# Performance work log

Measured on AMD Instinct MI355X. Metric: run time of the kernel, lower is better.

Reference implementation:

```python
import jax, jax.numpy as jnp
import numpy as np

N = 40000      # num nodes
E = 640000     # num edges (avg degree 16)
R = 4          # num relations
F = 128        # num_node_features
EMB = 128      # embedding_size
HID = 256      # hidden_size
V = 16         # direction_vocab_size
B = 4096       # number of (nest, food) queries


def setup_inputs() -> dict:
    key = jax.random.key(0)
    ks = jax.random.split(key, 17)
    s = 0.05
    return {
        "x": jax.random.normal(ks[0], (N, F), jnp.float32),
        "edge_index": jax.random.randint(ks[1], (2, E), 0, N, dtype=jnp.int32),
        "edge_type": jax.random.randint(ks[2], (E,), 0, R, dtype=jnp.int32),
        "nest_tensor": jax.random.randint(ks[3], (B,), 0, N, dtype=jnp.int32),
        "food_tensor": jax.random.randint(ks[4], (B,), 0, N, dtype=jnp.int32),
        # RGCN layer 1 (F -> EMB)
        "Wrel1": jax.random.normal(ks[5], (R, F, EMB), jnp.float32) * s,
        "Wroot1": jax.random.normal(ks[6], (F, EMB), jnp.float32) * s,
        "b1": jnp.zeros((EMB,), jnp.float32),
        # RGCN layer 2 (EMB -> EMB)
        "Wrel2": jax.random.normal(ks[7], (R, EMB, EMB), jnp.float32) * s,
        "Wroot2": jax.random.normal(ks[8], (EMB, EMB), jnp.float32) * s,
        "b2": jnp.zeros((EMB,), jnp.float32),
        # MLP heads
        "fc_W": jax.random.normal(ks[9], (2 * EMB, HID), jnp.float32) * s,
        "fc_b": jnp.zeros((HID,), jnp.float32),
        "dir_W": jax.random.normal(ks[10], (HID, V), jnp.float32) * s,
        "dir_b": jnp.zeros((V,), jnp.float32),
        "dist_W": jax.random.normal(ks[11], (HID, 1), jnp.float32) * s,
        "dist_b": jnp.zeros((1,), jnp.float32),
    }


def rgcn_conv(x, edge_index, edge_type, Wrel, Wroot, b, num_nodes):
    """PyG-style RGCNConv: root transform + per-relation mean-aggregated messages."""
    src, dst = edge_index[0], edge_index[1]
    out = x @ Wroot + b                                   # [N, H]
    num_rel = Wrel.shape[0]
    for r in range(num_rel):                              # small fixed loop over relations
        mask = (edge_type == r)
        xr = x @ Wrel[r]                                  # [N, H] transform-then-gather
        msg = jnp.where(mask[:, None], xr[src], 0.0)      # [E, H]
        agg = jax.ops.segment_sum(msg, dst, num_segments=num_nodes)
        cnt = jax.ops.segment_sum(mask.astype(x.dtype), dst, num_segments=num_nodes)
        out = out + agg / jnp.maximum(cnt, 1.0)[:, None]  # mean per relation per node
    return out


def reference(x, edge_index, edge_type, nest_tensor, food_tensor,
              Wrel1, Wroot1, b1, Wrel2, Wroot2, b2,
              fc_W, fc_b, dir_W, dir_b, dist_W, dist_b):
    num_nodes = x.shape[0]
    h = jax.nn.relu(rgcn_conv(x, edge_index, edge_type, Wrel1, Wroot1, b1, num_nodes))
    h = rgcn_conv(h, edge_index, edge_type, Wrel2, Wroot2, b2, num_nodes)
    combined = jnp.concatenate([h[nest_tensor], h[food_tensor]], axis=-1)  # [B, 2*EMB]
    hidden = jax.nn.relu(combined @ fc_W + fc_b)                           # [B, HID]
    token_a = jax.nn.log_softmax(hidden @ dir_W + dir_b, axis=-1)          # [B, V]
    token_b = hidden @ dist_W + dist_b                                     # [B, 1]
    return (token_a, token_b)
```

## Files before the change

kernel.cpp:

```cpp
#include <hip/hip_runtime.h>

#define N_NODES 40000
#define N_EDGES 640000
#define N_REL   4
#define NBINS   (N_NODES * N_REL)
#define EMB     128
#define HID     256
#define VOCAB   16
#define NB      4096
#define KTOT    640

typedef __attribute__((ext_vector_type(8))) short bf16x8;
typedef __attribute__((ext_vector_type(4))) float f32x4;

__device__ __forceinline__ short f2bf(float f) {
    union { float f; unsigned u; } x; x.f = f;
    unsigned r = x.u + 0x7fffu + ((x.u >> 16) & 1u);
    return (short)(r >> 16);
}
__device__ __forceinline__ float bf2f(short b) {
    union { unsigned u; float f; } x; x.u = ((unsigned)(unsigned short)b) << 16;
    return x.f;
}


__global__ __launch_bounds__(256) void hist_kernel(const int* __restrict__ ei,
                                                   const int* __restrict__ et,
                                                   int* __restrict__ bins) {
    int e = blockIdx.x * blockDim.x + threadIdx.x;
    if (e < N_EDGES) {
        int dst = ei[N_EDGES + e];
        int r   = et[e];
        atomicAdd(&bins[dst * N_REL + r], 1);
    }
}

__global__ __launch_bounds__(256) void scanA_kernel(const int* __restrict__ bins,
                                                    int* __restrict__ ptr,
                                                    int* __restrict__ bsum) {
    __shared__ int wsum[4];
    int t    = threadIdx.x;
    int base = blockIdx.x * 1024 + t * 4;
    int v[4];
#pragma unroll
    for (int i = 0; i < 4; ++i) {
        int idx = base + i;
        v[i] = (idx < NBINS) ? bins[idx] : 0;
    }
    int tot  = v[0] + v[1] + v[2] + v[3];
    int lane = t & 63, w = t >> 6;
    int inc  = tot;
#pragma unroll
    for (int d = 1; d < 64; d <<= 1) {
        int n = __shfl_up(inc, d);
        if (lane >= d) inc += n;
    }
    if (lane == 63) wsum[w] = inc;
    __syncthreads();
    int woff = 0;
    for (int i = 0; i < w; ++i) woff += wsum[i];
    int run = woff + inc - tot;
#pragma unroll
    for (int i = 0; i < 4; ++i) {
        int idx = base + i;
        if (idx < NBINS) ptr[idx] = run;
        run += v[i];
    }
    if (t == 255) bsum[blockIdx.x] = woff + inc;
}

__global__ __launch_bounds__(256) void scanB_kernel(const int* __restrict__ bsum,
                                                    int* __restrict__ boff, int nblk) {
    __shared__ int sh[256];
    int t = threadIdx.x;
    int v = (t < nblk) ? bsum[t] : 0;
    sh[t] = v;
    __syncthreads();
    for (int d = 1; d < 256; d <<= 1) {
        int n = (t >= d) ? sh[t - d] : 0;
        __syncthreads();
        sh[t] += n;
        __syncthreads();
    }
    if (t < nblk) boff[t] = sh[t] - v;
}

__global__ __launch_bounds__(256) void scanC_kernel(int* __restrict__ ptr,
                                                    int* __restrict__ cur,
                                                    const int* __restrict__ boff) {
    int base = blockIdx.x * 1024 + threadIdx.x * 4;
    int off  = boff[blockIdx.x];
#pragma unroll
    for (int i = 0; i < 4; ++i) {
        int idx = base + i;
        if (idx < NBINS) {
            int p = ptr[idx] + off;
            ptr[idx] = p;
            cur[idx] = p;
        }
    }
    if (blockIdx.x == 0 && threadIdx.x == 0) ptr[NBINS] = N_EDGES;
}

__global__ __launch_bounds__(256) void scatter_kernel(const int* __restrict__ ei,
                                                      const int* __restrict__ et,
                                                      int* __restrict__ cur,
                                                      int* __restrict__ perm) {
    int e = blockIdx.x * blockDim.x + threadIdx.x;
    if (e < N_EDGES) {
        int src = ei[e];
        int dst = ei[N_EDGES + e];
        int r   = et[e];
        int pos = atomicAdd(&cur[dst * N_REL + r], 1);
        perm[pos] = src;
    }
}

__global__ __launch_bounds__(256) void cvt_kernel(const float* __restrict__ in,
                                                  unsigned short* __restrict__ out) {
    int i = blockIdx.x * blockDim.x + threadIdx.x;
    float4 v = *reinterpret_cast<const float4*>(in + (size_t)i * 4);
    ushort4 o;
    o.x = (unsigned short)f2bf(v.x); o.y = (unsigned short)f2bf(v.y);
    o.z = (unsigned short)f2bf(v.z); o.w = (unsigned short)f2bf(v.w);
    *reinterpret_cast<ushort4*>(out + (size_t)i * 4) = o;
}

__global__ __launch_bounds__(256) void agg_csr_kernel(const unsigned short* __restrict__ Xb,
                                                      const int* __restrict__ ptr,
                                                      const int* __restrict__ perm,
                                                      float* __restrict__ S) {
    int node = blockIdx.x * 4 + (threadIdx.x >> 6);
    int l    = threadIdx.x & 63;

    int pr[5];
#pragma unroll
    for (int i = 0; i < 5; ++i) pr[i] = ptr[node * 4 + i];

    int wbase = pr[0];
    int srcs  = perm[min(wbase + l, N_EDGES - 1)];
    float* Sp = S + (size_t)node * 512 + l * 2;

#pragma unroll
    for (int r = 0; r < 4; ++r) {
        int s = pr[r], e = pr[r + 1];
        float ax = 0.f, ay = 0.f;
        for (int j = s; j < e; j += 4) {
            int hi = min(j + 3, e - 1);
            if (hi >= wbase + 64) {
                wbase = j;
                srcs  = perm[min(wbase + l, N_EDGES - 1)];
            }
            ushort2 v[4]; bool val[4];
#pragma unroll
            for (int u = 0; u < 4; ++u) {
                int jj = j + u;
                val[u] = jj < e;
                int src = __shfl(srcs, (val[u] ? jj : j) - wbase);
                v[u] = *reinterpret_cast<const ushort2*>(Xb + (size_t)src * 128 + l * 2);
            }
#pragma unroll
            for (int u = 0; u < 4; ++u) {
                ax += val[u] ? bf2f((short)v[u].x) : 0.f;
                ay += val[u] ? bf2f((short)v[u].y) : 0.f;
            }
        }
        float sc = 1.0f / (float)max(e - s, 1);
        *reinterpret_cast<float2*>(Sp + r * 128) = make_float2(ax * sc, ay * sc);
    }
}

__global__ __launch_bounds__(256) void prep_w(const float* __restrict__ Wroot,
                                              const float* __restrict__ Wrel,
                                              short* __restrict__ Wth,
                                              short* __restrict__ Wtl) {
    int col = blockIdx.x;
    for (int g = threadIdx.x; g < KTOT; g += 256) {
        float w = (g < 128) ? Wroot[(size_t)g * 128 + col]
                            : Wrel[(size_t)(g - 128) * 128 + col];
        short h  = f2bf(w);
        short lo = f2bf(w - bf2f(h));
        Wth[(size_t)col * KTOT + g] = h;
        Wtl[(size_t)col * KTOT + g] = lo;
    }
}

__global__ __launch_bounds__(256, 3) void gemm_layer_mfma(
        const float* __restrict__ X, const float* __restrict__ S,
        const short* __restrict__ Wth, const short* __restrict__ Wtl,
        const float* __restrict__ bias, float* __restrict__ C, int relu_out) {
    __shared__ __align__(16) short As_h[64 * 64];
    __shared__ __align__(16) short As_l[64 * 64];
    __shared__ __align__(16) short Bs_h[128 * 64];
    __shared__ __align__(16) short Bs_l[128 * 64];

    const int t   = threadIdx.x;
    const int rm  = blockIdx.x * 64;
    const int l   = t & 63, w = t >> 6;
    const int mh  = (w >> 1) * 32;
    const int nh  = (w & 1) * 64;
    const int r16 = l & 15, kch = l >> 4;

    f32x4 acc[2][4];
#pragma unroll
    for (int mt = 0; mt < 2; ++mt)
#pragma unroll
        for (int nt = 0; nt < 4; ++nt)
            acc[mt][nt] = (f32x4){0.f, 0.f, 0.f, 0.f};

    for (int kt = 0; kt < 10; ++kt) {
#pragma unroll
        for (int i = 0; i < 4; ++i) {
            int idx  = t + i * 256;
            int row  = idx >> 4;
            int kc   = (idx & 15) * 4;
            int grow = rm + row;
            float4 v;
            if (kt < 2) {
                v = *reinterpret_cast<const float4*>(X + (size_t)grow * 128 + kt * 64 + kc);
            } else {
                v = *reinterpret_cast<const float4*>(S + (size_t)grow * 512 + (kt - 2) * 64 + kc);
            }
            short h0 = f2bf(v.x), h1 = f2bf(v.y), h2 = f2bf(v.z), h3 = f2bf(v.w);
            short l0 = f2bf(v.x - bf2f(h0)), l1 = f2bf(v.y - bf2f(h1));
            short l2 = f2bf(v.z - bf2f(h2)), l3 = f2bf(v.w - bf2f(h3));
            int off = ((row << 7) + (kc << 1)) ^ ((row & 7) << 4);
            *reinterpret_cast<short4*>((char*)As_h + off) = make_short4(h0, h1, h2, h3);
            *reinterpret_cast<short4*>((char*)As_l + off) = make_short4(l0, l1, l2, l3);
        }
#pragma unroll
        for (int i = 0; i < 4; ++i) {
            int idx = t + i * 256;
            int col = idx >> 3;
            int k0  = (idx & 7) * 8;
            size_t goff = (size_t)col * KTOT + kt * 64 + k0;
            bf16x8 hv = *reinterpret_cast<const bf16x8*>(Wth + goff);
            bf16x8 lv = *reinterpret_cast<const bf16x8*>(Wtl + goff);
            int off = ((col << 7) + (k0 << 1)) ^ ((col & 7) << 4);
            *reinterpret_cast<bf16x8*>((char*)Bs_h + off) = hv;
            *reinterpret_cast<bf16x8*>((char*)Bs_l + off) = lv;
        }
        __syncthreads();
#pragma unroll
        for (int s = 0; s < 2; ++s) {
            int kb = s * 64 + kch * 16;
            bf16x8 ah[2], al[2], bh[4], bl[4];
#pragma unroll
            for (int mt = 0; mt < 2; ++mt) {
                int row = mh + mt * 16 + r16;
                int off = ((row << 7) + kb) ^ ((row & 7) << 4);
                ah[mt] = *reinterpret_cast<const bf16x8*>((const char*)As_h + off);
                al[mt] = *reinterpret_cast<const bf16x8*>((const char*)As_l + off);
            }
#pragma unroll
            for (int nt = 0; nt < 4; ++nt) {
                int col = nh + nt * 16 + r16;
                int off = ((col << 7) + kb) ^ ((col & 7) << 4);
                bh[nt] = *reinterpret_cast<const bf16x8*>((const char*)Bs_h + off);
                bl[nt] = *reinterpret_cast<const bf16x8*>((const char*)Bs_l + off);
            }
#pragma unroll
            for (int mt = 0; mt < 2; ++mt)
#pragma unroll
                for (int nt = 0; nt < 4; ++nt) {
                    acc[mt][nt] = __builtin_amdgcn_mfma_f32_16x16x32_bf16(ah[mt], bh[nt], acc[mt][nt], 0, 0, 0);
                    acc[mt][nt] = __builtin_amdgcn_mfma_f32_16x16x32_bf16(ah[mt], bl[nt], acc[mt][nt], 0, 0, 0);
                    acc[mt][nt] = __builtin_amdgcn_mfma_f32_16x16x32_bf16(al[mt], bh[nt], acc[mt][nt], 0, 0, 0);
                }
        }
        __syncthreads();
    }
#pragma unroll
    for (int mt = 0; mt < 2; ++mt)
#pragma unroll
        for (int nt = 0; nt < 4; ++nt) {
            int col = nh + nt * 16 + r16;
            float bv = bias[col];
#pragma unroll
            for (int r = 0; r < 4; ++r) {
                int row = rm + mh + mt * 16 + kch * 4 + r;
                float o = acc[mt][nt][r] + bv;
                if (relu_out) o = fmaxf(o, 0.f);
                C[(size_t)row * 128 + col] = o;
            }
        }
}

#define FMA16()                                                                 \
    acc[0][0] = fmaf(a0, b.x, acc[0][0]); acc[0][1] = fmaf(a0, b.y, acc[0][1]); \
    acc[0][2] = fmaf(a0, b.z, acc[0][2]); acc[0][3] = fmaf(a0, b.w, acc[0][3]); \
    acc[1][0] = fmaf(a1, b.x, acc[1][0]); acc[1][1] = fmaf(a1, b.y, acc[1][1]); \
    acc[1][2] = fmaf(a1, b.z, acc[1][2]); acc[1][3] = fmaf(a1, b.w, acc[1][3]); \
    acc[2][0] = fmaf(a2, b.x, acc[2][0]); acc[2][1] = fmaf(a2, b.y, acc[2][1]); \
    acc[2][2] = fmaf(a2, b.z, acc[2][2]); acc[2][3] = fmaf(a2, b.w, acc[2][3]); \
    acc[3][0] = fmaf(a3, b.x, acc[3][0]); acc[3][1] = fmaf(a3, b.y, acc[3][1]); \
    acc[3][2] = fmaf(a3, b.z, acc[3][2]); acc[3][3] = fmaf(a3, b.w, acc[3][3])

#define KSTEP(J, AX)                                                \
    {                                                               \
        float4 b  = bq##J;                                          \
        float  a0 = aq0.AX, a1 = aq1.AX, a2 = aq2.AX, a3 = aq3.AX;  \
        FMA16();                                                    \
    }

#define INNER_K128(AS, BS)                                                     \
    _Pragma("unroll 2")                                                        \
    for (int kk = 0; kk < 128; kk += 4) {                                      \
        float4 aq0 = *reinterpret_cast<const float4*>(&AS[ty * 4 + 0][kk]);    \
        float4 aq1 = *reinterpret_cast<const float4*>(&AS[ty * 4 + 1][kk]);    \
        float4 aq2 = *reinterpret_cast<const float4*>(&AS[ty * 4 + 2][kk]);    \
        float4 aq3 = *reinterpret_cast<const float4*>(&AS[ty * 4 + 3][kk]);    \
        float4 bq0 = *reinterpret_cast<const float4*>(&BS[kk + 0][tx * 4]);    \
        float4 bq1 = *reinterpret_cast<const float4*>(&BS[kk + 1][tx * 4]);    \
        float4 bq2 = *reinterpret_cast<const float4*>(&BS[kk + 2][tx * 4]);    \
        float4 bq3 = *reinterpret_cast<const float4*>(&BS[kk + 3][tx * 4]);    \
        KSTEP(0, x); KSTEP(1, y); KSTEP(2, z); KSTEP(3, w);                    \
    }

__global__ __launch_bounds__(256) void gemm_head(const float* __restrict__ H,
                                                 const int* __restrict__ nest,
                                                 const int* __restrict__ food,
                                                 const float* __restrict__ W,
                                                 const float* __restrict__ bias,
                                                 float* __restrict__ C) {
    __shared__ __align__(16) float As[64][132];
    __shared__ __align__(16) float Bs[128][68];
    int t  = threadIdx.x;
    int rm = blockIdx.x * 64;
    int cn = blockIdx.y * 64;
    int ty = t >> 4, tx = t & 15;
    float acc[4][4];
#pragma unroll
    for (int i = 0; i < 4; ++i)
#pragma unroll
        for (int j = 0; j < 4; ++j) acc[i][j] = 0.f;

    for (int kt = 0; kt < 2; ++kt) {
        const int* idx = (kt == 0) ? nest : food;
#pragma unroll
        for (int i = 0; i < 8; ++i) {
            int idx4 = t + i * 256;
            int row  = idx4 >> 5;
            int kc4  = idx4 & 31;
            int node = idx[rm + row];
            *reinterpret_cast<float4*>(&As[row][kc4 * 4]) =
                *reinterpret_cast<const float4*>(H + (size_t)node * 128 + kc4 * 4);
        }
#pragma unroll
        for (int i = 0; i < 8; ++i) {
            int idx4 = t + i * 256;
            int kk   = idx4 >> 4;
            int j4   = idx4 & 15;
            *reinterpret_cast<float4*>(&Bs[kk][j4 * 4]) =
                *reinterpret_cast<const float4*>(W + (size_t)(kt * 128 + kk) * 256 + cn + j4 * 4);
        }
        __syncthreads();
        INNER_K128(As, Bs);
        __syncthreads();
    }
    float4 bv = *reinterpret_cast<const float4*>(bias + cn + tx * 4);
#pragma unroll
    for (int i = 0; i < 4; ++i) {
        int grow = rm + ty * 4 + i;
        float4 o;
        o.x = fmaxf(acc[i][0] + bv.x, 0.f); o.y = fmaxf(acc[i][1] + bv.y, 0.f);
        o.z = fmaxf(acc[i][2] + bv.z, 0.f); o.w = fmaxf(acc[i][3] + bv.w, 0.f);
        *reinterpret_cast<float4*>(C + (size_t)grow * 256 + cn + tx * 4) = o;
    }
}

__global__ __launch_bounds__(256) void head_kernel(const float* __restrict__ hidden,
                                                   const float* __restrict__ dirW,
                                                   const float* __restrict__ dirB,
                                                   const float* __restrict__ distW,
                                                   const float* __restrict__ distB,
                                                   float* __restrict__ outA,
                                                   float* __restrict__ outB) {
    __shared__ __align__(16) float sm[4][256];
    int t = threadIdx.x;
    int w = t >> 6;
    int l = t & 63;
    int q = blockIdx.x * 4 + w;

    float4 hv = *reinterpret_cast<const float4*>(hidden + (size_t)q * 256 + l * 4);
    *reinterpret_cast<float4*>(&sm[w][l * 4]) = hv;
    __syncthreads();

    int v  = l & 15;
    int kc = l >> 4;
    float p = 0.f;
#pragma unroll
    for (int i = 0; i < 64; ++i) {
        int k = kc * 64 + i;
        p = fmaf(sm[w][k], dirW[k * VOCAB + v], p);
    }
    p += __shfl_xor(p, 16);
    p += __shfl_xor(p, 32);
    p += dirB[v];

    float m = p;
#pragma unroll
    for (int d = 1; d < 16; d <<= 1) m = fmaxf(m, __shfl_xor(m, d));
    float es = __expf(p - m);
    float ss = es;
#pragma unroll
    for (int d = 1; d < 16; d <<= 1) ss += __shfl_xor(ss, d);
    float outv = p - m - __logf(ss);
    if (l < 16) outA[(size_t)q * VOCAB + v] = outv;

    float pd = hv.x * distW[l * 4 + 0] + hv.y * distW[l * 4 + 1] +
               hv.z * distW[l * 4 + 2] + hv.w * distW[l * 4 + 3];
#pragma unroll
    for (int d = 1; d < 64; d <<= 1) pd += __shfl_xor(pd, d);
    if (l == 0) outB[q] = pd + distB[0];
}

extern "C" void kernel_launch(void* const* d_in, const int* in_sizes, int n_in,
                              void* d_out, int out_size, void* d_ws, size_t ws_size,
                              hipStream_t stream) {
    const float* x      = (const float*)d_in[0];
    const int*   ei     = (const int*)d_in[1];
    const int*   et     = (const int*)d_in[2];
    const int*   nest   = (const int*)d_in[3];
    const int*   food   = (const int*)d_in[4];
    const float* Wrel1  = (const float*)d_in[5];
    const float* Wroot1 = (const float*)d_in[6];
    const float* b1     = (const float*)d_in[7];
    const float* Wrel2  = (const float*)d_in[8];
    const float* Wroot2 = (const float*)d_in[9];
    const float* b2     = (const float*)d_in[10];
    const float* fcW    = (const float*)d_in[11];
    const float* fcB    = (const float*)d_in[12];
    const float* dirW   = (const float*)d_in[13];
    const float* dirB   = (const float*)d_in[14];
    const float* distW  = (const float*)d_in[15];
    const float* distB  = (const float*)d_in[16];

    char* ws = (char*)d_ws;
    size_t off = 0;
    auto alloc = [&](size_t bytes) {
        void* p = ws + off;
        off += (bytes + 255) & ~(size_t)255;
        return p;
    };
    float* S      = (float*)alloc((size_t)N_NODES * 512 * 4);
    float* hA     = (float*)alloc((size_t)N_NODES * 128 * 4);
    float* hB     = (float*)alloc((size_t)N_NODES * 128 * 4);
    float* hidden = (float*)alloc((size_t)NB * 256 * 4);
    short* wtbuf  = (short*)alloc((size_t)4 * 128 * KTOT * 2);
    int*   bins   = (int*)wtbuf;
    int*   ptr    = (int*)alloc((size_t)(NBINS + 1) * 4);
    int*   cur    = (int*)alloc((size_t)(NBINS + 1) * 4);
    int*   bsum   = (int*)alloc(256 * 4);
    int*   boff   = (int*)alloc(256 * 4);
    int*   perm   = (int*)alloc((size_t)N_EDGES * 4);

    unsigned short* xb = (unsigned short*)hB;

    short* wt1h = wtbuf;
    short* wt1l = wtbuf + 128 * KTOT;
    short* wt2h = wtbuf + 2 * 128 * KTOT;
    short* wt2l = wtbuf + 3 * 128 * KTOT;

    float* outA = (float*)d_out;
    float* outB = (float*)d_out + NB * 16;

    const int SCAN_BLKS = (NBINS + 1023) / 1024;
    const int CVT_BLKS  = (N_NODES * 128 / 4) / 256;

    hipMemsetAsync(bins, 0, (size_t)NBINS * 4, stream);
    hist_kernel<<<(N_EDGES + 255) / 256, 256, 0, stream>>>(ei, et, bins);
    scanA_kernel<<<SCAN_BLKS, 256, 0, stream>>>(bins, ptr, bsum);
    scanB_kernel<<<1, 256, 0, stream>>>(bsum, boff, SCAN_BLKS);
    scanC_kernel<<<SCAN_BLKS, 256, 0, stream>>>(ptr, cur, boff);
    scatter_kernel<<<(N_EDGES + 255) / 256, 256, 0, stream>>>(ei, et, cur, perm);

    prep_w<<<128, 256, 0, stream>>>(Wroot1, Wrel1, wt1h, wt1l);
    prep_w<<<128, 256, 0, stream>>>(Wroot2, Wrel2, wt2h, wt2l);

    cvt_kernel<<<CVT_BLKS, 256, 0, stream>>>(x, xb);
    agg_csr_kernel<<<N_NODES / 4, 256, 0, stream>>>(xb, ptr, perm, S);
    gemm_layer_mfma<<<625, 256, 0, stream>>>(x, S, wt1h, wt1l, b1, hA, 1);

    cvt_kernel<<<CVT_BLKS, 256, 0, stream>>>(hA, xb);
    agg_csr_kernel<<<N_NODES / 4, 256, 0, stream>>>(xb, ptr, perm, S);
    gemm_layer_mfma<<<625, 256, 0, stream>>>(hA, S, wt2h, wt2l, b2, hB, 0);

    gemm_head<<<dim3(64, 4), 256, 0, stream>>>(hB, nest, food, fcW, fcB, hidden);
    head_kernel<<<NB / 4, 256, 0, stream>>>(hidden, dirW, dirB, distW, distB, outA, outB);
}
```

Before: 334.5 us.

## Store aggregated messages in bf16, fuse layer-1 bf16 conversion, vectorize edge kernels

The per-relation mean-aggregated features S are now written as bf16 instead of fp32, which halves S traffic. The GEMM loads them directly into shared memory and drops the low-part split and the extra MFMA for that K range. The layer-1 GEMM epilogue also writes a bf16 copy of its output, removing a separate conversion kernel. The histogram and scatter kernels each process four edges per thread with int4 loads. Precision on the aggregated terms drops from split-bf16 (roughly fp32) to plain bf16.

```diff
diff --git a/kernel.cpp b/kernel.cpp
--- a/kernel.cpp
+++ b/kernel.cpp
@@ -27,12 +27,14 @@
 __global__ __launch_bounds__(256) void hist_kernel(const int* __restrict__ ei,
                                                    const int* __restrict__ et,
                                                    int* __restrict__ bins) {
-    int e = blockIdx.x * blockDim.x + threadIdx.x;
-    if (e < N_EDGES) {
-        int dst = ei[N_EDGES + e];
-        int r   = et[e];
-        atomicAdd(&bins[dst * N_REL + r], 1);
-    }
+    int e4 = (blockIdx.x * blockDim.x + threadIdx.x) * 4;
+    if (e4 >= N_EDGES) return;
+    int4 dst = *reinterpret_cast<const int4*>(ei + N_EDGES + e4);
+    int4 rr  = *reinterpret_cast<const int4*>(et + e4);
+    atomicAdd(&bins[dst.x * N_REL + rr.x], 1);
+    atomicAdd(&bins[dst.y * N_REL + rr.y], 1);
+    atomicAdd(&bins[dst.z * N_REL + rr.z], 1);
+    atomicAdd(&bins[dst.w * N_REL + rr.w], 1);
 }
 
 __global__ __launch_bounds__(256) void scanA_kernel(const int* __restrict__ bins,
@@ -106,14 +108,19 @@
                                                       const int* __restrict__ et,
                                                       int* __restrict__ cur,
                                                       int* __restrict__ perm) {
-    int e = blockIdx.x * blockDim.x + threadIdx.x;
-    if (e < N_EDGES) {
-        int src = ei[e];
-        int dst = ei[N_EDGES + e];
-        int r   = et[e];
-        int pos = atomicAdd(&cur[dst * N_REL + r], 1);
-        perm[pos] = src;
-    }
+    int e4 = (blockIdx.x * blockDim.x + threadIdx.x) * 4;
+    if (e4 >= N_EDGES) return;
+    int4 src = *reinterpret_cast<const int4*>(ei + e4);
+    int4 dst = *reinterpret_cast<const int4*>(ei + N_EDGES + e4);
+    int4 rr  = *reinterpret_cast<const int4*>(et + e4);
+    int p0 = atomicAdd(&cur[dst.x * N_REL + rr.x], 1);
+    int p1 = atomicAdd(&cur[dst.y * N_REL + rr.y], 1);
+    int p2 = atomicAdd(&cur[dst.z * N_REL + rr.z], 1);
+    int p3 = atomicAdd(&cur[dst.w * N_REL + rr.w], 1);
+    perm[p0] = src.x;
+    perm[p1] = src.y;
+    perm[p2] = src.z;
+    perm[p3] = src.w;
 }
 
 __global__ __launch_bounds__(256) void cvt_kernel(const float* __restrict__ in,
@@ -129,7 +136,7 @@
 __global__ __launch_bounds__(256) void agg_csr_kernel(const unsigned short* __restrict__ Xb,
                                                       const int* __restrict__ ptr,
                                                       const int* __restrict__ perm,
-                                                      float* __restrict__ S) {
+                                                      unsigned short* __restrict__ S) {
     int node = blockIdx.x * 4 + (threadIdx.x >> 6);
     int l    = threadIdx.x & 63;
 
@@ -139,7 +146,7 @@
 
     int wbase = pr[0];
     int srcs  = perm[min(wbase + l, N_EDGES - 1)];
-    float* Sp = S + (size_t)node * 512 + l * 2;
+    unsigned short* Sp = S + (size_t)node * 512 + l * 2;
 
 #pragma unroll
     for (int r = 0; r < 4; ++r) {
@@ -166,7 +173,10 @@
             }
         }
         float sc = 1.0f / (float)max(e - s, 1);
-        *reinterpret_cast<float2*>(Sp + r * 128) = make_float2(ax * sc, ay * sc);
+        ushort2 o;
+        o.x = (unsigned short)f2bf(ax * sc);
+        o.y = (unsigned short)f2bf(ay * sc);
+        *reinterpret_cast<ushort2*>(Sp + (size_t)r * 128) = o;
     }
 }
 
@@ -186,9 +196,10 @@
 }
 
 __global__ __launch_bounds__(256, 3) void gemm_layer_mfma(
-        const float* __restrict__ X, const float* __restrict__ S,
+        const float* __restrict__ X, const unsigned short* __restrict__ S,
         const short* __restrict__ Wth, const short* __restrict__ Wtl,
-        const float* __restrict__ bias, float* __restrict__ C, int relu_out) {
+        const float* __restrict__ bias, float* __restrict__ C,
+        unsigned short* __restrict__ Cb, int relu_out) {
     __shared__ __align__(16) short As_h[64 * 64];
     __shared__ __align__(16) short As_l[64 * 64];
     __shared__ __align__(16) short Bs_h[128 * 64];
@@ -209,24 +220,34 @@
             acc[mt][nt] = (f32x4){0.f, 0.f, 0.f, 0.f};
 
     for (int kt = 0; kt < 10; ++kt) {
-#pragma unroll
-        for (int i = 0; i < 4; ++i) {
-            int idx  = t + i * 256;
-            int row  = idx >> 4;
-            int kc   = (idx & 15) * 4;
-            int grow = rm + row;
-            float4 v;
-            if (kt < 2) {
-                v = *reinterpret_cast<const float4*>(X + (size_t)grow * 128 + kt * 64 + kc);
-            } else {
-                v = *reinterpret_cast<const float4*>(S + (size_t)grow * 512 + (kt - 2) * 64 + kc);
-            }
-            short h0 = f2bf(v.x), h1 = f2bf(v.y), h2 = f2bf(v.z), h3 = f2bf(v.w);
-            short l0 = f2bf(v.x - bf2f(h0)), l1 = f2bf(v.y - bf2f(h1));
-            short l2 = f2bf(v.z - bf2f(h2)), l3 = f2bf(v.w - bf2f(h3));
-            int off = ((row << 7) + (kc << 1)) ^ ((row & 7) << 4);
-            *reinterpret_cast<short4*>((char*)As_h + off) = make_short4(h0, h1, h2, h3);
-            *reinterpret_cast<short4*>((char*)As_l + off) = make_short4(l0, l1, l2, l3);
+        const bool xpart = (kt < 2);
+        if (xpart) {
+#pragma unroll
+            for (int i = 0; i < 4; ++i) {
+                int idx  = t + i * 256;
+                int row  = idx >> 4;
+                int kc   = (idx & 15) * 4;
+                int grow = rm + row;
+                float4 v = *reinterpret_cast<const float4*>(X + (size_t)grow * 128 + kt * 64 + kc);
+                short h0 = f2bf(v.x), h1 = f2bf(v.y), h2 = f2bf(v.z), h3 = f2bf(v.w);
+                short l0 = f2bf(v.x - bf2f(h0)), l1 = f2bf(v.y - bf2f(h1));
+                short l2 = f2bf(v.z - bf2f(h2)), l3 = f2bf(v.w - bf2f(h3));
+                int off = ((row << 7) + (kc << 1)) ^ ((row & 7) << 4);
+                *reinterpret_cast<short4*>((char*)As_h + off) = make_short4(h0, h1, h2, h3);
+                *reinterpret_cast<short4*>((char*)As_l + off) = make_short4(l0, l1, l2, l3);
+            }
+        } else {
+#pragma unroll
+            for (int i = 0; i < 2; ++i) {
+                int idx  = t + i * 256;
+                int row  = idx >> 3;
+                int k0   = (idx & 7) * 8;
+                int grow = rm + row;
+                bf16x8 v = *reinterpret_cast<const bf16x8*>(
+                    S + (size_t)grow * 512 + (kt - 2) * 64 + k0);
+                int off = ((row << 7) + (k0 << 1)) ^ ((row & 7) << 4);
+                *reinterpret_cast<bf16x8*>((char*)As_h + off) = v;
+            }
         }
 #pragma unroll
         for (int i = 0; i < 4; ++i) {
@@ -250,7 +271,8 @@
                 int row = mh + mt * 16 + r16;
                 int off = ((row << 7) + kb) ^ ((row & 7) << 4);
                 ah[mt] = *reinterpret_cast<const bf16x8*>((const char*)As_h + off);
-                al[mt] = *reinterpret_cast<const bf16x8*>((const char*)As_l + off);
+                if (xpart)
+                    al[mt] = *reinterpret_cast<const bf16x8*>((const char*)As_l + off);
             }
 #pragma unroll
             for (int nt = 0; nt < 4; ++nt) {
@@ -265,7 +287,8 @@
                 for (int nt = 0; nt < 4; ++nt) {
                     acc[mt][nt] = __builtin_amdgcn_mfma_f32_16x16x32_bf16(ah[mt], bh[nt], acc[mt][nt], 0, 0, 0);
                     acc[mt][nt] = __builtin_amdgcn_mfma_f32_16x16x32_bf16(ah[mt], bl[nt], acc[mt][nt], 0, 0, 0);
-                    acc[mt][nt] = __builtin_amdgcn_mfma_f32_16x16x32_bf16(al[mt], bh[nt], acc[mt][nt], 0, 0, 0);
+                    if (xpart)
+                        acc[mt][nt] = __builtin_amdgcn_mfma_f32_16x16x32_bf16(al[mt], bh[nt], acc[mt][nt], 0, 0, 0);
                 }
         }
         __syncthreads();
@@ -282,6 +305,7 @@
                 float o = acc[mt][nt][r] + bv;
                 if (relu_out) o = fmaxf(o, 0.f);
                 C[(size_t)row * 128 + col] = o;
+                if (Cb) Cb[(size_t)row * 128 + col] = (unsigned short)f2bf(o);
             }
         }
 }
@@ -443,7 +467,7 @@
         off += (bytes + 255) & ~(size_t)255;
         return p;
     };
-    float* S      = (float*)alloc((size_t)N_NODES * 512 * 4);
+    unsigned short* S = (unsigned short*)alloc((size_t)N_NODES * 512 * 2);
     float* hA     = (float*)alloc((size_t)N_NODES * 128 * 4);
     float* hB     = (float*)alloc((size_t)N_NODES * 128 * 4);
     float* hidden = (float*)alloc((size_t)NB * 256 * 4);
@@ -467,24 +491,24 @@
 
     const int SCAN_BLKS = (NBINS + 1023) / 1024;
     const int CVT_BLKS  = (N_NODES * 128 / 4) / 256;
+    const int E4_BLKS   = (N_EDGES / 4 + 255) / 256;
 
     hipMemsetAsync(bins, 0, (size_t)NBINS * 4, stream);
-    hist_kernel<<<(N_EDGES + 255) / 256, 256, 0, stream>>>(ei, et, bins);
+    hist_kernel<<<E4_BLKS, 256, 0, stream>>>(ei, et, bins);
     scanA_kernel<<<SCAN_BLKS, 256, 0, stream>>>(bins, ptr, bsum);
     scanB_kernel<<<1, 256, 0, stream>>>(bsum, boff, SCAN_BLKS);
     scanC_kernel<<<SCAN_BLKS, 256, 0, stream>>>(ptr, cur, boff);
-    scatter_kernel<<<(N_EDGES + 255) / 256, 256, 0, stream>>>(ei, et, cur, perm);
+    scatter_kernel<<<E4_BLKS, 256, 0, stream>>>(ei, et, cur, perm);
 
     prep_w<<<128, 256, 0, stream>>>(Wroot1, Wrel1, wt1h, wt1l);
     prep_w<<<128, 256, 0, stream>>>(Wroot2, Wrel2, wt2h, wt2l);
 
     cvt_kernel<<<CVT_BLKS, 256, 0, stream>>>(x, xb);
     agg_csr_kernel<<<N_NODES / 4, 256, 0, stream>>>(xb, ptr, perm, S);
-    gemm_layer_mfma<<<625, 256, 0, stream>>>(x, S, wt1h, wt1l, b1, hA, 1);
-
-    cvt_kernel<<<CVT_BLKS, 256, 0, stream>>>(hA, xb);
+    gemm_layer_mfma<<<625, 256, 0, stream>>>(x, S, wt1h, wt1l, b1, hA, xb, 1);
+
     agg_csr_kernel<<<N_NODES / 4, 256, 0, stream>>>(xb, ptr, perm, S);
-    gemm_layer_mfma<<<625, 256, 0, stream>>>(hA, S, wt2h, wt2l, b2, hB, 0);
+    gemm_layer_mfma<<<625, 256, 0, stream>>>(hA, S, wt2h, wt2l, b2, hB, (unsigned short*)nullptr, 0);
 
     gemm_head<<<dim3(64, 4), 256, 0, stream>>>(hB, nest, food, fcW, fcB, hidden);
     head_kernel<<<NB / 4, 256, 0, stream>>>(hidden, dirW, dirB, distW, distB, outA, outB);
```

After: 304.8 us. 1.1x faster.
